# Performance work log

Hardware: AMD Instinct MI355X
Metric: run time of the kernel (lower is better)

## Reference

```python
import jax, jax.numpy as jnp
import numpy as np

EPS = 1e-12


def setup_inputs() -> dict:
    key = jax.random.key(0)
    N, C, H, W = 32, 256, 56, 56
    k1, k2, k3 = jax.random.split(key, 3)
    x = jax.random.normal(k1, (N, C, H, W), dtype=jnp.float32)
    weight = 1.0 + 0.1 * jax.random.normal(k2, (C,), dtype=jnp.float32)
    bias = 0.1 * jax.random.normal(k3, (C,), dtype=jnp.float32)
    # Variable group sizes summing to C=256 (16 groups)
    gs = np.array([8, 24, 8, 16, 32, 16, 8, 8, 16, 24, 8, 16, 16, 8, 32, 16], dtype=np.int64)
    assert gs.sum() == C
    # Per-sample channel permutation expressed as row indices into x.view(N*C, H*W)
    rng = np.random.default_rng(0)
    perms = np.stack([rng.permutation(C) for _ in range(N)])  # [N, C]
    offs = np.arange(N)[:, None] * C
    indexes = (perms + offs).reshape(-1).astype(np.int64)
    inv = np.argsort(perms, axis=1)
    reverse_indexes = (inv + offs).reshape(-1).astype(np.int64)
    return {
        "x": x,
        "weight": weight,
        "bias": bias,
        "group_sizes": jnp.asarray(gs),
        "indexes": jnp.asarray(indexes),
        "reverse_indexes": jnp.asarray(reverse_indexes),
    }


def reference(x, weight, bias, group_sizes, indexes, reverse_indexes):
    N, C, H, W = x.shape
    HW = H * W
    gs = np.asarray(group_sizes)          # static group layout
    G = gs.shape[0]
    seg = jnp.asarray(np.repeat(np.arange(G), gs))  # [C] channel -> group id
    n = jnp.asarray(gs * HW, dtype=x.dtype)         # [G] elements per group

    # gather: per-sample channel permutation
    xg = x.reshape(N * C, HW)[indexes].reshape(N, C, HW)

    # per-group mean via segmented reduction over channels
    s1 = xg.sum(axis=2)                                    # [N, C]
    mu_g = jax.ops.segment_sum(s1.T, seg, num_segments=G).T / n      # [N, G]
    mu_c = mu_g[:, seg]                                    # [N, C]

    diff = xg - mu_c[:, :, None]
    s2 = (diff * diff).sum(axis=2)                         # [N, C]
    # torch.var default is unbiased -> divide by (n - 1)
    var_g = jax.ops.segment_sum(s2.T, seg, num_segments=G).T / (n - 1.0)
    ivar_c = (1.0 / jnp.sqrt(var_g + EPS))[:, seg]         # [N, C]

    out = diff * ivar_c[:, :, None] * weight[None, :, None] + bias[None, :, None]

    # scatter back to original channel order
    out = out.reshape(N * C, HW)[reverse_indexes].reshape(N, C, H, W)
    return out
```

## Files before the change

### kernel.cpp

```cpp
#include <hip/hip_runtime.h>

#define N_ 32
#define C_ 256
#define G_ 16
#define HW_ 3136
#define HW4_ 784
#define EPS_ 1e-12f

__device__ __forceinline__ int rd_int(const int* __restrict__ p, int i, bool is64) {
    return is64 ? p[2 * i] : p[i];
}

__device__ __forceinline__ int group_of(const int* __restrict__ gs, int j, bool is64) {
    int g = 0, P = 0;
    #pragma unroll
    for (int k = 0; k < G_; k++) {
        P += rd_int(gs, k, is64);
        if (j >= P) g++;
    }
    return g;
}

__global__ __launch_bounds__(256) void vgn_reduce(
    const float* __restrict__ x,
    const int*   __restrict__ indexes,
    const int*   __restrict__ group_sizes,
    float*       __restrict__ gsums)
{
    const bool is64 = (group_sizes[1] == 0);

    const int row = blockIdx.x;
    const int n   = row >> 8;
    const int j   = row & 255;
    const int src = rd_int(indexes, row, is64);

    const float4* x4 = (const float4*)(x + (size_t)src * HW_);

    float s = 0.f, s2 = 0.f;
    for (int i = threadIdx.x; i < HW4_; i += 256) {
        float4 v = x4[i];
        s  += v.x + v.y + v.z + v.w;
        s2 += v.x * v.x + v.y * v.y + v.z * v.z + v.w * v.w;
    }

    #pragma unroll
    for (int off = 32; off > 0; off >>= 1) {
        s  += __shfl_down(s,  off);
        s2 += __shfl_down(s2, off);
    }

    __shared__ float ls[4], ls2[4];
    const int wave = threadIdx.x >> 6;
    if ((threadIdx.x & 63) == 0) { ls[wave] = s; ls2[wave] = s2; }
    __syncthreads();

    if (threadIdx.x == 0) {
        float S  = ls[0]  + ls[1]  + ls[2]  + ls[3];
        float S2 = ls2[0] + ls2[1] + ls2[2] + ls2[3];
        const int g = group_of(group_sizes, j, is64);
        atomicAdd(&gsums[(n * G_ + g) * 2 + 0], S);
        atomicAdd(&gsums[(n * G_ + g) * 2 + 1], S2);
    }
}

__global__ __launch_bounds__(256) void vgn_norm(
    const float* __restrict__ x,
    const int*   __restrict__ indexes,
    const int*   __restrict__ group_sizes,
    const float* __restrict__ weight,
    const float* __restrict__ bias,
    const float* __restrict__ gsums,
    float*       __restrict__ out)
{
    const bool is64 = (group_sizes[1] == 0);

    const int row = blockIdx.x;
    const int n   = row >> 8;
    const int j   = row & 255;
    const int src = rd_int(indexes, row, is64);

    const int g   = group_of(group_sizes, j, is64);
    const int gsz = rd_int(group_sizes, g, is64);
    const float cnt = (float)(gsz * HW_);

    const float S   = gsums[(n * G_ + g) * 2 + 0];
    const float S2  = gsums[(n * G_ + g) * 2 + 1];
    const float mu  = S / cnt;
    const float var = (S2 - mu * S) / (cnt - 1.0f);
    const float ivr = rsqrtf(var + EPS_);

    const float scale = ivr * weight[j];
    const float shift = bias[j] - mu * scale;

    const float4* x4 = (const float4*)(x   + (size_t)src * HW_);
    float4*       o4 = (float4*)      (out + (size_t)src * HW_);

    for (int i = threadIdx.x; i < HW4_; i += 256) {
        float4 v = x4[i];
        float4 r;
        r.x = v.x * scale + shift;
        r.y = v.y * scale + shift;
        r.z = v.z * scale + shift;
        r.w = v.w * scale + shift;
        o4[i] = r;
    }
}

extern "C" void kernel_launch(void* const* d_in, const int* in_sizes, int n_in,
                              void* d_out, int out_size, void* d_ws, size_t ws_size,
                              hipStream_t stream) {
    const float* x           = (const float*)d_in[0];
    const float* weight      = (const float*)d_in[1];
    const float* bias        = (const float*)d_in[2];
    const int*   group_sizes = (const int*)  d_in[3];
    const int*   indexes     = (const int*)  d_in[4];

    float* gsums = (float*)d_ws;

    hipMemsetAsync(gsums, 0, N_ * G_ * 2 * sizeof(float), stream);

    dim3 grid(N_ * C_), block(256);
    vgn_reduce<<<grid, block, 0, stream>>>(x, indexes, group_sizes, gsums);
    vgn_norm  <<<grid, block, 0, stream>>>(x, indexes, group_sizes,
                                           weight, bias, gsums, (float*)d_out);
}
```

Measured before the change: 208.4 us.

## Replace group atomics with per-row partials reduced in norm kernel; nontemporal stores

The reduce kernel now writes per-row sum and sum-of-squares to workspace instead of atomically accumulating per-group totals. The norm kernel has one wave gather the rows of its group and shuffle-reduce them. This removes the memset launch and the atomic contention. Output stores become nontemporal to avoid polluting cache. In exchange every norm block repeats a small group reduction and adds a block barrier.

```diff
diff --git a/kernel.cpp b/kernel.cpp
--- a/kernel.cpp
+++ b/kernel.cpp
@@ -7,38 +7,28 @@
 #define HW4_ 784
 #define EPS_ 1e-12f
 
+typedef float vf4 __attribute__((ext_vector_type(4)));
+
 __device__ __forceinline__ int rd_int(const int* __restrict__ p, int i, bool is64) {
     return is64 ? p[2 * i] : p[i];
-}
-
-__device__ __forceinline__ int group_of(const int* __restrict__ gs, int j, bool is64) {
-    int g = 0, P = 0;
-    #pragma unroll
-    for (int k = 0; k < G_; k++) {
-        P += rd_int(gs, k, is64);
-        if (j >= P) g++;
-    }
-    return g;
 }
 
 __global__ __launch_bounds__(256) void vgn_reduce(
     const float* __restrict__ x,
     const int*   __restrict__ indexes,
     const int*   __restrict__ group_sizes,
-    float*       __restrict__ gsums)
+    float*       __restrict__ rsums)
 {
     const bool is64 = (group_sizes[1] == 0);
 
     const int row = blockIdx.x;
-    const int n   = row >> 8;
-    const int j   = row & 255;
     const int src = rd_int(indexes, row, is64);
 
-    const float4* x4 = (const float4*)(x + (size_t)src * HW_);
+    const vf4* x4 = (const vf4*)(x + (size_t)src * HW_);
 
     float s = 0.f, s2 = 0.f;
     for (int i = threadIdx.x; i < HW4_; i += 256) {
-        float4 v = x4[i];
+        vf4 v = x4[i];
         s  += v.x + v.y + v.z + v.w;
         s2 += v.x * v.x + v.y * v.y + v.z * v.z + v.w * v.w;
     }
@@ -55,11 +45,8 @@
     __syncthreads();
 
     if (threadIdx.x == 0) {
-        float S  = ls[0]  + ls[1]  + ls[2]  + ls[3];
-        float S2 = ls2[0] + ls2[1] + ls2[2] + ls2[3];
-        const int g = group_of(group_sizes, j, is64);
-        atomicAdd(&gsums[(n * G_ + g) * 2 + 0], S);
-        atomicAdd(&gsums[(n * G_ + g) * 2 + 1], S2);
+        rsums[row * 2 + 0] = ls[0]  + ls[1]  + ls[2]  + ls[3];
+        rsums[row * 2 + 1] = ls2[0] + ls2[1] + ls2[2] + ls2[3];
     }
 }
 
@@ -69,7 +56,7 @@
     const int*   __restrict__ group_sizes,
     const float* __restrict__ weight,
     const float* __restrict__ bias,
-    const float* __restrict__ gsums,
+    const float* __restrict__ rsums,
     float*       __restrict__ out)
 {
     const bool is64 = (group_sizes[1] == 0);
@@ -79,12 +66,34 @@
     const int j   = row & 255;
     const int src = rd_int(indexes, row, is64);
 
-    const int g   = group_of(group_sizes, j, is64);
+    int g = 0, P = 0, Pg = 0;
+    #pragma unroll
+    for (int k = 0; k < G_; k++) {
+        P += rd_int(group_sizes, k, is64);
+        if (j >= P) { g++; Pg = P; }
+    }
     const int gsz = rd_int(group_sizes, g, is64);
+
+    __shared__ float sS, sS2;
+    if (threadIdx.x < 64) {
+        float a = 0.f, b = 0.f;
+        if (threadIdx.x < gsz) {
+            const int pr = (n * C_ + Pg + threadIdx.x) * 2;
+            a = rsums[pr + 0];
+            b = rsums[pr + 1];
+        }
+        #pragma unroll
+        for (int off = 32; off > 0; off >>= 1) {
+            a += __shfl_down(a, off);
+            b += __shfl_down(b, off);
+        }
+        if (threadIdx.x == 0) { sS = a; sS2 = b; }
+    }
+    __syncthreads();
+
     const float cnt = (float)(gsz * HW_);
-
-    const float S   = gsums[(n * G_ + g) * 2 + 0];
-    const float S2  = gsums[(n * G_ + g) * 2 + 1];
+    const float S   = sS;
+    const float S2  = sS2;
     const float mu  = S / cnt;
     const float var = (S2 - mu * S) / (cnt - 1.0f);
     const float ivr = rsqrtf(var + EPS_);
@@ -92,17 +101,17 @@
     const float scale = ivr * weight[j];
     const float shift = bias[j] - mu * scale;
 
-    const float4* x4 = (const float4*)(x   + (size_t)src * HW_);
-    float4*       o4 = (float4*)      (out + (size_t)src * HW_);
+    const vf4* x4 = (const vf4*)(x   + (size_t)src * HW_);
+    vf4*       o4 = (vf4*)      (out + (size_t)src * HW_);
 
     for (int i = threadIdx.x; i < HW4_; i += 256) {
-        float4 v = x4[i];
-        float4 r;
+        vf4 v = x4[i];
+        vf4 r;
         r.x = v.x * scale + shift;
         r.y = v.y * scale + shift;
         r.z = v.z * scale + shift;
         r.w = v.w * scale + shift;
-        o4[i] = r;
+        __builtin_nontemporal_store(r, &o4[i]);
     }
 }
 
@@ -115,12 +124,10 @@
     const int*   group_sizes = (const int*)  d_in[3];
     const int*   indexes     = (const int*)  d_in[4];
 
-    float* gsums = (float*)d_ws;
-
-    hipMemsetAsync(gsums, 0, N_ * G_ * 2 * sizeof(float), stream);
+    float* rsums = (float*)d_ws;
 
     dim3 grid(N_ * C_), block(256);
-    vgn_reduce<<<grid, block, 0, stream>>>(x, indexes, group_sizes, gsums);
+    vgn_reduce<<<grid, block, 0, stream>>>(x, indexes, group_sizes, rsums);
     vgn_norm  <<<grid, block, 0, stream>>>(x, indexes, group_sizes,
-                                           weight, bias, gsums, (float*)d_out);
+                                           weight, bias, rsums, (float*)d_out);
 }
```

Result: faster. 200.8 us (-3.6%).
